# Kernel optimization log

Measured on AMD Instinct MI355X. Metric: run time of the kernel, lower is better.

Reference implementation:

```python
import jax, jax.numpy as jnp
import numpy as np

D_MODEL = 512  # = sub_length = seq_length (last axis of x)


def make_overlap_mask(S, n, m):
    # Faithful to MultiHeadSelfAttentiondis.create_mask:
    # True where 0.5 <= overlap_ratio < 1, or i == j. (The ratio>=1 elif branch is dead code.)
    d = np.abs(np.arange(S)[:, None] - np.arange(S)[None, :])
    overlap = np.maximum(0, m - d * n)
    ratio = overlap / float(m)
    mask = ((ratio >= 0.5) & (ratio < 1.0)) | (d == 0)
    return jnp.asarray(mask)


def setup_inputs() -> dict:
    key = jax.random.key(0)
    k1, k2, k3 = jax.random.split(key, 3)
    B, D, S, L = 16, 8, 256, D_MODEL
    x = jax.random.normal(k1, (B, D, S, L), dtype=jnp.float32)
    # nn.Linear(d_model, 3*d_model): weight [3L, L], bias [3L]
    Wqkv = jax.random.normal(k2, (3 * L, L), dtype=jnp.float32) / np.sqrt(L)
    bqkv = jax.random.normal(k3, (3 * L,), dtype=jnp.float32) * 0.01
    return {"x": x, "Wqkv": Wqkv, "bqkv": bqkv, "n": 256}


def reference(x, Wqkv, bqkv, n):
    B, D, S, L = x.shape
    mask = make_overlap_mask(S, n, L)  # [S, S] bool, static
    # Shared QKV projection, batched over all channels at once (replaces the per-dim loop)
    qkv = jnp.einsum('bdsl,fl->bdsf', x, Wqkv) + bqkv  # [B, D, S, 3L]
    q, k, v = jnp.split(qkv, 3, axis=-1)               # each [B, D, S, L]
    scores = jnp.einsum('bdsl,bdtl->bdst', q, k) / jnp.sqrt(jnp.float32(L))
    attn = jax.nn.softmax(scores, axis=-1)             # [B, D, S, S]
    # masked_fill(mask, 0) happens AFTER softmax in the original
    attn = jnp.where(mask[None, None], 0.0, attn)
    out = jnp.einsum('bdst,bdtl->bdsl', attn, v)       # [B, D, S, L]
    output = out.reshape(B, D * S, L)
    # Block-diagonal attention matrix: block d is attn[:, d]
    eyeD = jnp.eye(D, dtype=attn.dtype)
    big = eyeD[None, :, None, :, None] * attn[:, :, :, None, :]  # [B, D, S, D, S]
    output_matrix_attn = big.reshape(B, D * S, D * S)
    return output, output_matrix_attn
```

## Files before the change

### kernel.cpp

```cpp
#include <hip/hip_runtime.h>
#include <hip/hip_bf16.h>
#include <cstdint>


typedef unsigned short u16;
typedef short bf16x8 __attribute__((ext_vector_type(8)));
typedef float f32x4 __attribute__((ext_vector_type(4)));

__device__ __forceinline__ u16 f2bf(float f) {
    union { float f; unsigned int u; } v; v.f = f;
    unsigned int r = v.u + 0x7FFF + ((v.u >> 16) & 1);
    return (u16)(r >> 16);
}

__device__ __forceinline__ void gload16(const u16* g, u16* l) {
    __builtin_amdgcn_global_load_lds(
        (const __attribute__((address_space(1))) unsigned int*)g,
        (__attribute__((address_space(3))) unsigned int*)l, 16, 0, 0);
}

__device__ __forceinline__ f32x4 mfma16(bf16x8 a, bf16x8 b, f32x4 c) {
    return __builtin_amdgcn_mfma_f32_16x16x32_bf16(a, b, c, 0, 0, 0);
}

__global__ __launch_bounds__(256) void cast_bf16(const float* __restrict__ x,
                                                 const float* __restrict__ w,
                                                 u16* __restrict__ xb,
                                                 u16* __restrict__ wb) {
    const size_t NX = 16777216 / 8, NW = 786432 / 8;
    size_t i = (size_t)blockIdx.x * 256 + threadIdx.x;
    const float* src; u16* dst; size_t e;
    if (i < NX)            { src = x; dst = xb; e = i; }
    else if (i < NX + NW)  { src = w; dst = wb; e = i - NX; }
    else return;
    const float4 a = *(const float4*)&src[e * 8];
    const float4 b = *(const float4*)&src[e * 8 + 4];
    u16 o[8] = { f2bf(a.x), f2bf(a.y), f2bf(a.z), f2bf(a.w),
                 f2bf(b.x), f2bf(b.y), f2bf(b.z), f2bf(b.w) };
    *(uint4*)&dst[e * 8] = *(const uint4*)o;
}

__global__ __launch_bounds__(256, 2) void qkv_gemm(const u16* __restrict__ xb,
                                                   const u16* __restrict__ wb,
                                                   const float* __restrict__ bias,
                                                   u16* __restrict__ qk,
                                                   u16* __restrict__ vt) {
    __shared__ __align__(16) u16 sA[8 * 512];
    __shared__ __align__(16) u16 sB[16 * 512];
    const int tid = threadIdx.x, lane = tid & 63, w = tid >> 6;
    const int lr = lane & 15, lh = lane >> 4;
    const int f0 = blockIdx.x * 256, m0 = blockIdx.y * 128;
    const int wm = w & 1, wf = w >> 1;

    f32x4 acc[4][8];
#pragma unroll
    for (int i = 0; i < 4; ++i)
#pragma unroll
        for (int j = 0; j < 8; ++j) acc[i][j] = (f32x4){0.f, 0.f, 0.f, 0.f};

    for (int k0 = 0; k0 < 512; k0 += 32) {
#pragma unroll
        for (int i = 0; i < 6; ++i) {
            const int j = w * 6 + i;
            if (j < 8) {
                gload16(xb + (size_t)(m0 + j * 16 + lr) * 512 + k0 + lh * 8,
                        &sA[j * 512]);
            } else {
                const int jb = j - 8;
                gload16(wb + (size_t)(f0 + jb * 16 + lr) * 512 + k0 + lh * 8,
                        &sB[jb * 512]);
            }
        }
        __syncthreads();
        bf16x8 af[4], bf[8];
#pragma unroll
        for (int mt = 0; mt < 4; ++mt)
            af[mt] = *(const bf16x8*)&sA[(wm * 4 + mt) * 512 + lane * 8];
#pragma unroll
        for (int ft = 0; ft < 8; ++ft)
            bf[ft] = *(const bf16x8*)&sB[(wf * 8 + ft) * 512 + lane * 8];
#pragma unroll
        for (int mt = 0; mt < 4; ++mt)
#pragma unroll
            for (int ft = 0; ft < 8; ++ft)
                acc[mt][ft] = mfma16(af[mt], bf[ft], acc[mt][ft]);
        __syncthreads();
    }

    const bool isV = (f0 >= 1024);
#pragma unroll
    for (int ft = 0; ft < 8; ++ft) {
        const int f = f0 + wf * 128 + ft * 16 + lr;
        const float bv = bias[f];
#pragma unroll
        for (int mt = 0; mt < 4; ++mt) {
            const int mbase = m0 + wm * 64 + mt * 16 + lh * 4;
            const f32x4 a = acc[mt][ft];
            if (!isV) {
#pragma unroll
                for (int r = 0; r < 4; ++r)
                    qk[(size_t)(mbase + r) * 1024 + f] = f2bf(a[r] + bv);
            } else {
                const int nn = f - 1024;
                const int bd = mbase >> 8, t = mbase & 255;
                ushort4 pk;
                pk.x = f2bf(a[0] + bv); pk.y = f2bf(a[1] + bv);
                pk.z = f2bf(a[2] + bv); pk.w = f2bf(a[3] + bv);
                *(ushort4*)&vt[(size_t)bd * 131072 + (size_t)nn * 256 + t] = pk;
            }
        }
    }
}

#define HS 136
#define MT 552
#define KS 4432
__global__ __launch_bounds__(256, 1) void attn_kernel(const u16* __restrict__ qk,
                                                      const u16* __restrict__ vt,
                                                      const int* __restrict__ n_ptr,
                                                      float* __restrict__ out,
                                                      float* __restrict__ outmat) {
    __shared__ __align__(16) u16 sQ[8 * 512];
    __shared__ __align__(16) u16 sK[16 * 512];
    __shared__ __align__(16) u16 sP[8 * KS];
    __shared__ float sStat[128][2];

    const int tid = threadIdx.x, lane = tid & 63, w = tid >> 6;
    const int lr = lane & 15, lh = lane >> 4;
    const int r0 = blockIdx.x * 128, bd = blockIdx.y;
    const int n = *n_ptr;
    const int wm = w & 1, wt = w >> 1;
    const size_t qbase = (size_t)bd * 256 * 1024;

    f32x4 acc[4][8];
#pragma unroll
    for (int i = 0; i < 4; ++i)
#pragma unroll
        for (int j = 0; j < 8; ++j) acc[i][j] = (f32x4){0.f, 0.f, 0.f, 0.f};

    for (int k0 = 0; k0 < 512; k0 += 32) {
#pragma unroll
        for (int i = 0; i < 6; ++i) {
            const int j = w * 6 + i;
            if (j < 8) {
                gload16(qk + qbase + (size_t)(r0 + j * 16 + lr) * 1024 + k0 + lh * 8,
                        &sQ[j * 512]);
            } else {
                const int jb = j - 8;
                gload16(qk + qbase + (size_t)(jb * 16 + lr) * 1024 + 512 + k0 + lh * 8,
                        &sK[jb * 512]);
            }
        }
        __syncthreads();
        bf16x8 af[4], bf[8];
#pragma unroll
        for (int mt = 0; mt < 4; ++mt)
            af[mt] = *(const bf16x8*)&sQ[(wm * 4 + mt) * 512 + lane * 8];
#pragma unroll
        for (int jt = 0; jt < 8; ++jt)
            bf[jt] = *(const bf16x8*)&sK[(wt * 8 + jt) * 512 + lane * 8];
#pragma unroll
        for (int mt = 0; mt < 4; ++mt)
#pragma unroll
            for (int jt = 0; jt < 8; ++jt)
                acc[mt][jt] = mfma16(af[mt], bf[jt], acc[mt][jt]);
        __syncthreads();
    }

    const float scale = 0.044194173824159216f;
#pragma unroll
    for (int i = 0; i < 4; ++i)
#pragma unroll
        for (int j = 0; j < 8; ++j) acc[i][j] *= scale;

    float rmax[4][4], rinv[4][4];
#pragma unroll
    for (int i = 0; i < 4; ++i)
#pragma unroll
        for (int r = 0; r < 4; ++r) {
            float v = -1e30f;
#pragma unroll
            for (int j = 0; j < 8; ++j) v = fmaxf(v, acc[i][j][r]);
            v = fmaxf(v, __shfl_xor(v, 1));
            v = fmaxf(v, __shfl_xor(v, 2));
            v = fmaxf(v, __shfl_xor(v, 4));
            v = fmaxf(v, __shfl_xor(v, 8));
            if (lr == 0) sStat[wm * 64 + i * 16 + lh * 4 + r][wt] = v;
        }
    __syncthreads();
#pragma unroll
    for (int i = 0; i < 4; ++i)
#pragma unroll
        for (int r = 0; r < 4; ++r) {
            const int m = wm * 64 + i * 16 + lh * 4 + r;
            rmax[i][r] = fmaxf(sStat[m][0], sStat[m][1]);
        }
    __syncthreads();
#pragma unroll
    for (int i = 0; i < 4; ++i)
#pragma unroll
        for (int r = 0; r < 4; ++r) {
            float s = 0.f;
#pragma unroll
            for (int j = 0; j < 8; ++j) {
                const float p = __expf(acc[i][j][r] - rmax[i][r]);
                acc[i][j][r] = p;
                s += p;
            }
            s += __shfl_xor(s, 1);
            s += __shfl_xor(s, 2);
            s += __shfl_xor(s, 4);
            s += __shfl_xor(s, 8);
            if (lr == 0) sStat[wm * 64 + i * 16 + lh * 4 + r][wt] = s;
        }
    __syncthreads();
#pragma unroll
    for (int i = 0; i < 4; ++i)
#pragma unroll
        for (int r = 0; r < 4; ++r) {
            const int m = wm * 64 + i * 16 + lh * 4 + r;
            rinv[i][r] = 1.0f / (sStat[m][0] + sStat[m][1]);
        }

    const int b_ = bd >> 3, dd = bd & 7;
#pragma unroll
    for (int i = 0; i < 4; ++i)
#pragma unroll
        for (int r = 0; r < 4; ++r) {
            const int m_loc = wm * 64 + i * 16 + lh * 4 + r;
            const int ig = r0 + m_loc;
            float* orow = &outmat[(size_t)b_ * 4194304 +
                                  (size_t)(dd * 256 + ig) * 2048 + dd * 256];
#pragma unroll
            for (int j = 0; j < 8; ++j) {
                const int t = wt * 128 + j * 16 + lr;
                float a = acc[i][j][r] * rinv[i][r];
                const int d = (ig > t) ? (ig - t) : (t - ig);
                int ov = 512 - d * n; if (ov < 0) ov = 0;
                if (d == 0 || ((2 * ov >= 512) && (ov < 512))) a = 0.f;
                orow[t] = a;
                sP[(t >> 5) * KS + (m_loc >> 4) * MT + ((t >> 3) & 3) * HS +
                   (m_loc & 15) * 8 + (t & 7)] = f2bf(a);
            }
        }
    __syncthreads();

    const int wn = wt;
#pragma unroll 1
    for (int nc = 0; nc < 2; ++nc) {
#pragma unroll
        for (int i = 0; i < 4; ++i)
#pragma unroll
            for (int j = 0; j < 8; ++j) acc[i][j] = (f32x4){0.f, 0.f, 0.f, 0.f};
#pragma unroll 1
        for (int t0 = 0; t0 < 256; t0 += 32) {
#pragma unroll
            for (int i = 0; i < 4; ++i) {
                const int nt = w * 4 + i;
                const int n_g = nc * 256 + nt * 16 + lr;
                gload16(vt + (size_t)bd * 131072 + (size_t)n_g * 256 + t0 + lh * 8,
                        &sK[nt * 512]);
            }
            __syncthreads();
            bf16x8 af[4], bf[8];
            const int kstep = t0 >> 5;
#pragma unroll
            for (int mt = 0; mt < 4; ++mt)
                af[mt] = *(const bf16x8*)&sP[kstep * KS + (wm * 4 + mt) * MT +
                                             lh * HS + lr * 8];
#pragma unroll
            for (int jt = 0; jt < 8; ++jt)
                bf[jt] = *(const bf16x8*)&sK[(wn * 8 + jt) * 512 + lane * 8];
#pragma unroll
            for (int mt = 0; mt < 4; ++mt)
#pragma unroll
                for (int jt = 0; jt < 8; ++jt)
                    acc[mt][jt] = mfma16(af[mt], bf[jt], acc[mt][jt]);
            __syncthreads();
        }
#pragma unroll
        for (int mt = 0; mt < 4; ++mt)
#pragma unroll
            for (int jt = 0; jt < 8; ++jt) {
                const int ng = nc * 256 + wn * 128 + jt * 16 + lr;
#pragma unroll
                for (int r = 0; r < 4; ++r) {
                    const int m_loc = wm * 64 + mt * 16 + lh * 4 + r;
                    out[((size_t)bd * 256 + r0 + m_loc) * 512 + ng] = acc[mt][jt][r];
                }
            }
    }
}

extern "C" void kernel_launch(void* const* d_in, const int* in_sizes, int n_in,
                              void* d_out, int out_size, void* d_ws, size_t ws_size,
                              hipStream_t stream) {
    (void)in_sizes; (void)n_in; (void)out_size; (void)ws_size;
    const float* x     = (const float*)d_in[0];
    const float* Wqkv  = (const float*)d_in[1];
    const float* bqkv  = (const float*)d_in[2];
    const int*   n_ptr = (const int*)d_in[3];

    float* out    = (float*)d_out;
    float* outmat = out + (size_t)16 * 2048 * 512;

    u16* xb = (u16*)d_ws;
    u16* wb = xb + 16777216;
    u16* qk = wb + 786432;
    u16* vt = qk + (size_t)33554432;

    hipMemsetAsync(outmat, 0, (size_t)16 * 2048 * 2048 * sizeof(float), stream);

    cast_bf16<<<8576, 256, 0, stream>>>(x, Wqkv, xb, wb);

    dim3 g1(6, 256);
    qkv_gemm<<<g1, 256, 0, stream>>>(xb, wb, bqkv, qk, vt);

    dim3 g2(2, 128);
    attn_kernel<<<g2, 256, 0, stream>>>(qk, vt, n_ptr, out, outmat);
}
```

Baseline: 538.6 us.

## Store Q/K/V in MFMA-fragment tiled layout and fuse zero-fill into attention

```diff
diff --git a/kernel.cpp b/kernel.cpp
--- a/kernel.cpp
+++ b/kernel.cpp
@@ -43,8 +43,9 @@
 __global__ __launch_bounds__(256, 2) void qkv_gemm(const u16* __restrict__ xb,
                                                    const u16* __restrict__ wb,
                                                    const float* __restrict__ bias,
-                                                   u16* __restrict__ qk,
-                                                   u16* __restrict__ vt) {
+                                                   u16* __restrict__ qb,
+                                                   u16* __restrict__ kb,
+                                                   u16* __restrict__ vb) {
     __shared__ __align__(16) u16 sA[8 * 512];
     __shared__ __align__(16) u16 sB[16 * 512];
     const int tid = threadIdx.x, lane = tid & 63, w = tid >> 6;
@@ -58,6 +59,7 @@
 #pragma unroll
         for (int j = 0; j < 8; ++j) acc[i][j] = (f32x4){0.f, 0.f, 0.f, 0.f};
 
+#pragma unroll 1
     for (int k0 = 0; k0 < 512; k0 += 32) {
 #pragma unroll
         for (int i = 0; i < 6; ++i) {
@@ -87,80 +89,117 @@
         __syncthreads();
     }
 
-    const bool isV = (f0 >= 1024);
-#pragma unroll
-    for (int ft = 0; ft < 8; ++ft) {
-        const int f = f0 + wf * 128 + ft * 16 + lr;
-        const float bv = bias[f];
-#pragma unroll
-        for (int mt = 0; mt < 4; ++mt) {
-            const int mbase = m0 + wm * 64 + mt * 16 + lh * 4;
-            const f32x4 a = acc[mt][ft];
-            if (!isV) {
-#pragma unroll
-                for (int r = 0; r < 4; ++r)
-                    qk[(size_t)(mbase + r) * 1024 + f] = f2bf(a[r] + bv);
-            } else {
-                const int nn = f - 1024;
-                const int bd = mbase >> 8, t = mbase & 255;
-                ushort4 pk;
-                pk.x = f2bf(a[0] + bv); pk.y = f2bf(a[1] + bv);
-                pk.z = f2bf(a[2] + bv); pk.w = f2bf(a[3] + bv);
-                *(ushort4*)&vt[(size_t)bd * 131072 + (size_t)nn * 256 + t] = pk;
-            }
-        }
+    u16* patch = &sA[w * 1024];
+    const int bdq = m0 >> 8;
+    float bv[8];
+#pragma unroll
+    for (int ft = 0; ft < 8; ++ft) bv[ft] = bias[f0 + wf * 128 + ft * 16 + lr];
+
+    if (f0 < 1024) {
+        u16* dstb = (f0 < 512) ? qb : kb;
+        const int mtileg = ((m0 & 255) >> 4) + wm * 4;
+        const int kbase = ((f0 & 511) + wf * 128) >> 5;
+#pragma unroll
+        for (int mt = 0; mt < 4; ++mt)
+#pragma unroll
+            for (int ftp = 0; ftp < 4; ++ftp) {
+#pragma unroll
+                for (int h = 0; h < 2; ++h) {
+                    const int ft = ftp * 2 + h;
+                    const f32x4 a = acc[mt][ft];
+#pragma unroll
+                    for (int r = 0; r < 4; ++r)
+                        patch[(lh * 4 + r) * 40 + h * 16 + lr] = f2bf(a[r] + bv[ft]);
+                }
+                asm volatile("s_waitcnt lgkmcnt(0)" ::: "memory");
+                bf16x8 frag = *(const bf16x8*)&patch[lr * 40 + lh * 8];
+                u16* dst = dstb +
+                    ((size_t)(bdq * 16 + mtileg + mt) * 16 + (kbase + ftp)) * 512 +
+                    lane * 8;
+                *(bf16x8*)dst = frag;
+            }
+    } else {
+        const int nbase = ((f0 - 1024) >> 4) + wf * 8;
+        const int tbase = ((m0 & 255) >> 5) + wm * 2;
+#pragma unroll
+        for (int ft = 0; ft < 8; ++ft)
+#pragma unroll
+            for (int mtp = 0; mtp < 2; ++mtp) {
+#pragma unroll
+                for (int h = 0; h < 2; ++h) {
+                    const f32x4 a = acc[mtp * 2 + h][ft];
+#pragma unroll
+                    for (int r = 0; r < 4; ++r)
+                        patch[lr * 40 + h * 16 + lh * 4 + r] = f2bf(a[r] + bv[ft]);
+                }
+                asm volatile("s_waitcnt lgkmcnt(0)" ::: "memory");
+                bf16x8 frag = *(const bf16x8*)&patch[lr * 40 + lh * 8];
+                u16* dst = vb +
+                    ((size_t)(bdq * 32 + nbase + ft) * 8 + (tbase + mtp)) * 512 +
+                    lane * 8;
+                *(bf16x8*)dst = frag;
+            }
     }
 }
 
-#define HS 136
-#define MT 552
-#define KS 4432
-__global__ __launch_bounds__(256, 1) void attn_kernel(const u16* __restrict__ qk,
-                                                      const u16* __restrict__ vt,
+__global__ __launch_bounds__(256, 2) void attn_kernel(const u16* __restrict__ qb,
+                                                      const u16* __restrict__ kb,
+                                                      const u16* __restrict__ vb,
                                                       const int* __restrict__ n_ptr,
                                                       float* __restrict__ out,
                                                       float* __restrict__ outmat) {
-    __shared__ __align__(16) u16 sQ[8 * 512];
+    __shared__ __align__(16) u16 sQ[4 * 512];
     __shared__ __align__(16) u16 sK[16 * 512];
-    __shared__ __align__(16) u16 sP[8 * KS];
-    __shared__ float sStat[128][2];
+    __shared__ __align__(16) u16 sP[8 * 4 * 512];
+    __shared__ float sStat[64][2];
 
     const int tid = threadIdx.x, lane = tid & 63, w = tid >> 6;
     const int lr = lane & 15, lh = lane >> 4;
-    const int r0 = blockIdx.x * 128, bd = blockIdx.y;
+    const int r0 = blockIdx.x * 64, bd = blockIdx.y;
     const int n = *n_ptr;
     const int wm = w & 1, wt = w >> 1;
-    const size_t qbase = (size_t)bd * 256 * 1024;
-
-    f32x4 acc[4][8];
-#pragma unroll
-    for (int i = 0; i < 4; ++i)
+    const int b_ = bd >> 3, dd = bd & 7;
+    float* zbase = &outmat[(size_t)b_ * 4194304 + (size_t)(dd * 256 + r0) * 2048];
+    const float4 f4z = make_float4(0.f, 0.f, 0.f, 0.f);
+
+    f32x4 acc[2][8];
+#pragma unroll
+    for (int i = 0; i < 2; ++i)
 #pragma unroll
         for (int j = 0; j < 8; ++j) acc[i][j] = (f32x4){0.f, 0.f, 0.f, 0.f};
 
+#pragma unroll 1
     for (int k0 = 0; k0 < 512; k0 += 32) {
-#pragma unroll
-        for (int i = 0; i < 6; ++i) {
-            const int j = w * 6 + i;
-            if (j < 8) {
-                gload16(qk + qbase + (size_t)(r0 + j * 16 + lr) * 1024 + k0 + lh * 8,
-                        &sQ[j * 512]);
+        const int kc = k0 >> 5;
+#pragma unroll
+        for (int i = 0; i < 5; ++i) {
+            const int j = w * 5 + i;
+            if (j < 4) {
+                gload16(qb + ((size_t)(bd * 16 + blockIdx.x * 4 + j) * 16 + kc) * 512 +
+                        lane * 8, &sQ[j * 512]);
             } else {
-                const int jb = j - 8;
-                gload16(qk + qbase + (size_t)(jb * 16 + lr) * 1024 + 512 + k0 + lh * 8,
+                const int jb = j - 4;
+                gload16(kb + ((size_t)(bd * 16 + jb) * 16 + kc) * 512 + lane * 8,
                         &sK[jb * 512]);
             }
         }
+#pragma unroll
+        for (int u = 0; u < 8; ++u) {
+            const int idx = (kc * 8 + u) * 256 + tid;
+            const int row = idx >> 9, c4 = idx & 511;
+            if ((c4 >> 6) != dd)
+                *(float4*)&zbase[(size_t)row * 2048 + c4 * 4] = f4z;
+        }
         __syncthreads();
-        bf16x8 af[4], bf[8];
-#pragma unroll
-        for (int mt = 0; mt < 4; ++mt)
-            af[mt] = *(const bf16x8*)&sQ[(wm * 4 + mt) * 512 + lane * 8];
+        bf16x8 af[2], bf[8];
+#pragma unroll
+        for (int mt = 0; mt < 2; ++mt)
+            af[mt] = *(const bf16x8*)&sQ[(wm * 2 + mt) * 512 + lane * 8];
 #pragma unroll
         for (int jt = 0; jt < 8; ++jt)
             bf[jt] = *(const bf16x8*)&sK[(wt * 8 + jt) * 512 + lane * 8];
 #pragma unroll
-        for (int mt = 0; mt < 4; ++mt)
+        for (int mt = 0; mt < 2; ++mt)
 #pragma unroll
             for (int jt = 0; jt < 8; ++jt)
                 acc[mt][jt] = mfma16(af[mt], bf[jt], acc[mt][jt]);
@@ -169,13 +208,13 @@
 
     const float scale = 0.044194173824159216f;
 #pragma unroll
-    for (int i = 0; i < 4; ++i)
+    for (int i = 0; i < 2; ++i)
 #pragma unroll
         for (int j = 0; j < 8; ++j) acc[i][j] *= scale;
 
-    float rmax[4][4], rinv[4][4];
-#pragma unroll
-    for (int i = 0; i < 4; ++i)
+    float rmax[2][4], rinv[2][4];
+#pragma unroll
+    for (int i = 0; i < 2; ++i)
 #pragma unroll
         for (int r = 0; r < 4; ++r) {
             float v = -1e30f;
@@ -185,19 +224,19 @@
             v = fmaxf(v, __shfl_xor(v, 2));
             v = fmaxf(v, __shfl_xor(v, 4));
             v = fmaxf(v, __shfl_xor(v, 8));
-            if (lr == 0) sStat[wm * 64 + i * 16 + lh * 4 + r][wt] = v;
+            if (lr == 0) sStat[wm * 32 + i * 16 + lh * 4 + r][wt] = v;
         }
     __syncthreads();
 #pragma unroll
-    for (int i = 0; i < 4; ++i)
-#pragma unroll
-        for (int r = 0; r < 4; ++r) {
-            const int m = wm * 64 + i * 16 + lh * 4 + r;
+    for (int i = 0; i < 2; ++i)
+#pragma unroll
+        for (int r = 0; r < 4; ++r) {
+            const int m = wm * 32 + i * 16 + lh * 4 + r;
             rmax[i][r] = fmaxf(sStat[m][0], sStat[m][1]);
         }
     __syncthreads();
 #pragma unroll
-    for (int i = 0; i < 4; ++i)
+    for (int i = 0; i < 2; ++i)
 #pragma unroll
         for (int r = 0; r < 4; ++r) {
             float s = 0.f;
@@ -211,23 +250,22 @@
             s += __shfl_xor(s, 2);
             s += __shfl_xor(s, 4);
             s += __shfl_xor(s, 8);
-            if (lr == 0) sStat[wm * 64 + i * 16 + lh * 4 + r][wt] = s;
+            if (lr == 0) sStat[wm * 32 + i * 16 + lh * 4 + r][wt] = s;
         }
     __syncthreads();
 #pragma unroll
-    for (int i = 0; i < 4; ++i)
-#pragma unroll
-        for (int r = 0; r < 4; ++r) {
-            const int m = wm * 64 + i * 16 + lh * 4 + r;
+    for (int i = 0; i < 2; ++i)
+#pragma unroll
+        for (int r = 0; r < 4; ++r) {
+            const int m = wm * 32 + i * 16 + lh * 4 + r;
             rinv[i][r] = 1.0f / (sStat[m][0] + sStat[m][1]);
         }
 
-    const int b_ = bd >> 3, dd = bd & 7;
-#pragma unroll
-    for (int i = 0; i < 4; ++i)
-#pragma unroll
-        for (int r = 0; r < 4; ++r) {
-            const int m_loc = wm * 64 + i * 16 + lh * 4 + r;
+#pragma unroll
+    for (int i = 0; i < 2; ++i)
+#pragma unroll
+        for (int r = 0; r < 4; ++r) {
+            const int m_loc = wm * 32 + i * 16 + lh * 4 + r;
             const int ig = r0 + m_loc;
             float* orow = &outmat[(size_t)b_ * 4194304 +
                                   (size_t)(dd * 256 + ig) * 2048 + dd * 256];
@@ -239,53 +277,50 @@
                 int ov = 512 - d * n; if (ov < 0) ov = 0;
                 if (d == 0 || ((2 * ov >= 512) && (ov < 512))) a = 0.f;
                 orow[t] = a;
-                sP[(t >> 5) * KS + (m_loc >> 4) * MT + ((t >> 3) & 3) * HS +
-                   (m_loc & 15) * 8 + (t & 7)] = f2bf(a);
+                sP[((t >> 5) * 4 + (m_loc >> 4)) * 512 +
+                   (((t & 31) >> 3) * 16 + (m_loc & 15)) * 8 + (t & 7)] = f2bf(a);
             }
         }
     __syncthreads();
 
-    const int wn = wt;
 #pragma unroll 1
     for (int nc = 0; nc < 2; ++nc) {
 #pragma unroll
-        for (int i = 0; i < 4; ++i)
+        for (int i = 0; i < 2; ++i)
 #pragma unroll
             for (int j = 0; j < 8; ++j) acc[i][j] = (f32x4){0.f, 0.f, 0.f, 0.f};
 #pragma unroll 1
         for (int t0 = 0; t0 < 256; t0 += 32) {
+            const int tc = t0 >> 5;
 #pragma unroll
             for (int i = 0; i < 4; ++i) {
                 const int nt = w * 4 + i;
-                const int n_g = nc * 256 + nt * 16 + lr;
-                gload16(vt + (size_t)bd * 131072 + (size_t)n_g * 256 + t0 + lh * 8,
-                        &sK[nt * 512]);
+                gload16(vb + ((size_t)(bd * 32 + nc * 16 + nt) * 8 + tc) * 512 +
+                        lane * 8, &sK[nt * 512]);
             }
             __syncthreads();
-            bf16x8 af[4], bf[8];
-            const int kstep = t0 >> 5;
-#pragma unroll
-            for (int mt = 0; mt < 4; ++mt)
-                af[mt] = *(const bf16x8*)&sP[kstep * KS + (wm * 4 + mt) * MT +
-                                             lh * HS + lr * 8];
+            bf16x8 af[2], bf[8];
+#pragma unroll
+            for (int mt = 0; mt < 2; ++mt)
+                af[mt] = *(const bf16x8*)&sP[(tc * 4 + wm * 2 + mt) * 512 + lane * 8];
 #pragma unroll
             for (int jt = 0; jt < 8; ++jt)
-                bf[jt] = *(const bf16x8*)&sK[(wn * 8 + jt) * 512 + lane * 8];
-#pragma unroll
-            for (int mt = 0; mt < 4; ++mt)
+                bf[jt] = *(const bf16x8*)&sK[(wt * 8 + jt) * 512 + lane * 8];
+#pragma unroll
+            for (int mt = 0; mt < 2; ++mt)
 #pragma unroll
                 for (int jt = 0; jt < 8; ++jt)
                     acc[mt][jt] = mfma16(af[mt], bf[jt], acc[mt][jt]);
             __syncthreads();
         }
 #pragma unroll
-        for (int mt = 0; mt < 4; ++mt)
+        for (int mt = 0; mt < 2; ++mt)
 #pragma unroll
             for (int jt = 0; jt < 8; ++jt) {
-                const int ng = nc * 256 + wn * 128 + jt * 16 + lr;
+                const int ng = nc * 256 + wt * 128 + jt * 16 + lr;
 #pragma unroll
                 for (int r = 0; r < 4; ++r) {
-                    const int m_loc = wm * 64 + mt * 16 + lh * 4 + r;
+                    const int m_loc = wm * 32 + mt * 16 + lh * 4 + r;
                     out[((size_t)bd * 256 + r0 + m_loc) * 512 + ng] = acc[mt][jt][r];
                 }
             }
@@ -306,16 +341,15 @@
 
     u16* xb = (u16*)d_ws;
     u16* wb = xb + 16777216;
-    u16* qk = wb + 786432;
-    u16* vt = qk + (size_t)33554432;
-
-    hipMemsetAsync(outmat, 0, (size_t)16 * 2048 * 2048 * sizeof(float), stream);
+    u16* qb = wb + 786432;
+    u16* kb = qb + 16777216;
+    u16* vb = kb + 16777216;
 
     cast_bf16<<<8576, 256, 0, stream>>>(x, Wqkv, xb, wb);
 
     dim3 g1(6, 256);
-    qkv_gemm<<<g1, 256, 0, stream>>>(xb, wb, bqkv, qk, vt);
-
-    dim3 g2(2, 128);
-    attn_kernel<<<g2, 256, 0, stream>>>(qk, vt, n_ptr, out, outmat);
-}
+    qkv_gemm<<<g1, 256, 0, stream>>>(xb, wb, bqkv, qb, kb, vb);
+
+    dim3 g2(4, 128);
+    attn_kernel<<<g2, 256, 0, stream>>>(qb, kb, vb, n_ptr, out, outmat);
+}
```

New measurement: 515.4 us. -4.3%, faster.
